# Kernel optimization log

Hardware: AMD Instinct MI355X
Metric: run time of the kernel (lower is better)

## Reference

```python
import jax, jax.numpy as jnp
import numpy as np

IH, IW = 32, 32
HEADS = 8
DIM_HEAD = 32
INNER = HEADS * DIM_HEAD  # 256
INP = 256
OUP = 256
SCALE = DIM_HEAD ** -0.5


def _relative_index(ih, iw):
    # Reproduce the torch buffer computation (meshgrid indexing='ij').
    yy, xx = np.meshgrid(np.arange(ih), np.arange(iw), indexing='ij')
    coords = np.stack([yy.ravel(), xx.ravel()])            # [2, n]
    rel = coords[:, :, None] - coords[:, None, :]          # [2, n, n]
    rel[0] += ih - 1
    rel[1] += iw - 1
    rel[0] *= 2 * iw - 1
    idx = rel.sum(0).ravel()                               # [n*n]
    return jnp.asarray(idx, dtype=jnp.int32)


def setup_inputs() -> dict:
    key = jax.random.key(0)
    k1, k2, k3, k4 = jax.random.split(key, 4)
    B, N = 16, IH * IW
    x = jax.random.normal(k1, (B, N, INP), dtype=jnp.float32)
    # Parameters (stored as [in, out] so forward is x @ W).
    W_qkv = jax.random.normal(k2, (INP, 3 * INNER), dtype=jnp.float32) * 0.02
    W_out = jax.random.normal(k3, (INNER, OUP), dtype=jnp.float32) * 0.02
    b_out = jnp.zeros((OUP,), dtype=jnp.float32)
    bias_table = jax.random.normal(k4, ((2 * IH - 1) * (2 * IW - 1), HEADS), dtype=jnp.float32) * 0.02
    rel_index = _relative_index(IH, IW)
    return {"x": x, "W_qkv": W_qkv, "W_out": W_out, "b_out": b_out,
            "bias_table": bias_table, "rel_index": rel_index}


def reference(x, W_qkv, W_out, b_out, bias_table, rel_index):
    B, N, _ = x.shape
    qkv = x @ W_qkv                                        # [B, N, 3*inner]
    q, k, v = jnp.split(qkv, 3, axis=-1)
    def to_heads(t):  # b n (h d) -> b h n d
        return t.reshape(B, N, HEADS, DIM_HEAD).transpose(0, 2, 1, 3)
    q, k, v = to_heads(q), to_heads(k), to_heads(v)
    dots = jnp.einsum('bhnd,bhmd->bhnm', q, k) * SCALE     # [B, H, N, N]
    # Gather relative position bias: [n*n, heads] -> [1, heads, n, n]
    rel_bias = bias_table[rel_index].reshape(N, N, HEADS).transpose(2, 0, 1)
    dots = dots + rel_bias[None]
    attn = jax.nn.softmax(dots, axis=-1)
    out = jnp.einsum('bhnm,bhmd->bhnd', attn, v)           # [B, H, N, D]
    out = out.transpose(0, 2, 1, 3).reshape(B, N, INNER)   # b n (h d)
    return out @ W_out + b_out
```

## Files before the change

kernel.cpp:

```cpp
#include <hip/hip_runtime.h>
#include <stdint.h>
#include <stddef.h>


typedef _Float16 f16;
typedef __attribute__((ext_vector_type(8))) _Float16 half8;
typedef __attribute__((ext_vector_type(4))) _Float16 half4;
typedef __attribute__((ext_vector_type(2))) __fp16 fp16x2;
typedef __attribute__((ext_vector_type(4))) float f32x4;

#define MFMA16(a, b, c) __builtin_amdgcn_mfma_f32_16x16x32_f16((a), (b), (c), 0, 0, 0)

__global__ __launch_bounds__(256) void prep_kernel(
    const float* __restrict__ x,
    const float* __restrict__ W_qkv, const float* __restrict__ W_out,
    const float* __restrict__ bias_table, const int* __restrict__ rel_index,
    f16* __restrict__ Wtq, f16* __restrict__ Wto, f16* __restrict__ ebC,
    f16* __restrict__ xh)
{
  (void)rel_index;
  const float kLog2e = 1.4426950408889634f;
  const float kScale = 0.17677669529663687f * kLog2e;
  int tid = blockIdx.x * 256 + threadIdx.x;
  if (tid < 24576) {
    int c = tid >> 5;
    int k8 = (tid & 31) << 3;
    float s = (c < 256) ? kScale : 1.0f;
    f16* dst = Wtq + c * 256 + k8;
#pragma unroll
    for (int j = 0; j < 8; ++j)
      dst[j] = (f16)(W_qkv[(k8 + j) * 768 + c] * s);
  } else if (tid < 32768) {
    int t = tid - 24576;
    int c = t >> 5;
    int k8 = (t & 31) << 3;
    f16* dst = Wto + c * 256 + k8;
#pragma unroll
    for (int j = 0; j < 8; ++j)
      dst[j] = (f16)W_out[(k8 + j) * 256 + c];
  } else if (tid < 97280) {
    int t = tid - 32768;
    int e = t * 8;
    int h = e / 64512;
    int r = e - h * 64512;
    int dy = r >> 10;
    int xi = (r >> 5) & 31;
    int xj0 = r & 31;
    int base = dy * 63 + xi + 31;
    f16* dst = ebC + e;
#pragma unroll
    for (int j = 0; j < 8; ++j)
      dst[j] = (f16)__expf(bias_table[(base - (xj0 + j)) * 8 + h]);
  } else {
    int t = tid - 97280;
    const float* src = x + (size_t)t * 8;
    f16* dst = xh + (size_t)t * 8;
#pragma unroll
    for (int j = 0; j < 8; ++j) dst[j] = (f16)src[j];
  }
}

__global__ __launch_bounds__(256, 4) void qkv_kernel(
    const f16* __restrict__ xh, const f16* __restrict__ Wt,
    f16* __restrict__ Qh, f16* __restrict__ Kh, f16* __restrict__ Vt)
{
  __shared__ f16 Bs[64 * 256];
  int mt = blockIdx.x, nt = blockIdx.y;
  int tid = threadIdx.x;
  int wave = tid >> 6, lane = tid & 63;
  int g = lane >> 4, q16 = lane & 15;
  int cbase = nt * 64;
  char* BsB = (char*)Bs;
  const f16* WtG = Wt + (size_t)cbase * 256;
#pragma unroll
  for (int i = 0; i < 8; ++i) {
    int c = i * 256 + tid;
    int row = c >> 5;
    int colb = (c & 31) << 4;
    half8 v = *(const half8*)(WtG + c * 8);
    *(half8*)(BsB + row * 512 + (colb ^ ((row & 7) << 4))) = v;
  }
  __syncthreads();

  int rbase = mt * 256 + wave * 64;
  const f16* xr0 = xh + (size_t)(rbase + q16) * 256 + g * 8;
  f32x4 acc[4][4] = {};
#pragma unroll 2
  for (int kc = 0; kc < 8; ++kc) {
    half8 bf[4];
#pragma unroll
    for (int cf = 0; cf < 4; ++cf) {
      int row = cf * 16 + q16;
      int colb = kc * 64 + g * 16;
      bf[cf] = *(const half8*)(BsB + row * 512 + (colb ^ ((row & 7) << 4)));
    }
#pragma unroll
    for (int mf = 0; mf < 4; ++mf) {
      half8 af = *(const half8*)(xr0 + (size_t)(mf * 16) * 256 + kc * 32);
#pragma unroll
      for (int cf = 0; cf < 4; ++cf)
        acc[mf][cf] = MFMA16(af, bf[cf], acc[mf][cf]);
    }
  }

#pragma unroll
  for (int mf = 0; mf < 4; ++mf) {
#pragma unroll
    for (int cf = 0; cf < 4; ++cf) {
      int c = cbase + cf * 16 + q16;
      int which = c >> 8, h = (c >> 5) & 7, d = c & 31;
      int m0 = rbase + mf * 16 + g * 4;
      int b = m0 >> 10, n0 = m0 & 1023;
      size_t bh = (size_t)(b * 8 + h);
      if (which == 2) {
        half4 vv;
#pragma unroll
        for (int r = 0; r < 4; ++r) vv[r] = (f16)acc[mf][cf][r];
        *(half4*)(Vt + (((bh << 5) | d) << 10) + n0) = vv;
      } else {
        f16* base = (which == 0) ? Qh : Kh;
#pragma unroll
        for (int r = 0; r < 4; ++r)
          base[((bh << 10) | (n0 + r)) * 32 + d] = (f16)acc[mf][cf][r];
      }
    }
  }
}

__global__ __launch_bounds__(256) void attn_kernel(
    const f16* __restrict__ Qh, const f16* __restrict__ Kh,
    const f16* __restrict__ Vt, const f16* __restrict__ ebC,
    f16* __restrict__ Oh)
{
  int bid = blockIdx.x;
  int h = bid & 7;
  int rest = bid >> 3;
  int qt = rest & 3;
  int b = rest >> 2;
  int wave = threadIdx.x >> 6, lane = threadIdx.x & 63;
  int g = lane >> 4, q16 = lane & 15;
  int bh = b * 8 + h;
  int qbase = qt * 256 + wave * 64;
  const f16* Qb = Qh + ((size_t)bh << 15);
  const f16* Kb = Kh + ((size_t)bh << 15);
  const f16* Vb = Vt + ((size_t)bh << 15);

  half8 qf0 = *(const half8*)(Qb + (size_t)(qbase +  0 + q16) * 32 + g * 8);
  half8 qf1 = *(const half8*)(Qb + (size_t)(qbase + 16 + q16) * 32 + g * 8);
  half8 qf2 = *(const half8*)(Qb + (size_t)(qbase + 32 + q16) * 32 + g * 8);
  half8 qf3 = *(const half8*)(Qb + (size_t)(qbase + 48 + q16) * 32 + g * 8);

  int kr0 = ((q16 >> 2) << 3) | (q16 & 3);
  const f16* Kp0 = Kb + kr0 * 32 + g * 8;
  const f16* Kp1 = Kp0 + 4 * 32;
  const f16* Vp0 = Vb + (size_t)q16 * 1024 + g * 8;
  const f16* Vp1 = Vb + (size_t)(16 + q16) * 1024 + g * 8;
  int yi0 = qbase >> 5;
  const f16* Bp = ebC + ((((h * 63 + yi0 + 31) * 32 + q16) << 5) + g * 8);

  f32x4 o0a = {0.f,0.f,0.f,0.f}, o1a = {0.f,0.f,0.f,0.f};
  f32x4 o0b = {0.f,0.f,0.f,0.f}, o1b = {0.f,0.f,0.f,0.f};
  f32x4 o0c = {0.f,0.f,0.f,0.f}, o1c = {0.f,0.f,0.f,0.f};
  f32x4 o0d = {0.f,0.f,0.f,0.f}, o1d = {0.f,0.f,0.f,0.f};
  float lsa = 0.f, lsb = 0.f, lsc = 0.f, lsd = 0.f;
  const fp16x2 one2 = {(__fp16)1.0f, (__fp16)1.0f};
  (void)one2;

#if __has_builtin(__builtin_amdgcn_fdot2)
#define LSUM(LS, PU)                                                         \
    LS = __builtin_amdgcn_fdot2(PU.h2[0], one2, LS, false);                  \
    LS = __builtin_amdgcn_fdot2(PU.h2[1], one2, LS, false);                  \
    LS = __builtin_amdgcn_fdot2(PU.h2[2], one2, LS, false);                  \
    LS = __builtin_amdgcn_fdot2(PU.h2[3], one2, LS, false);
#else
#define LSUM(LS, PU)                                                         \
    _Pragma("unroll") for (int i = 0; i < 8; ++i) { LS += (float)PU.h8[i]; }
#endif

#define FRAG_BODY(QF, K0, K1, V0, V1, EB, O0, O1, LS)                        \
  {                                                                          \
    const f32x4 zz = {0.f, 0.f, 0.f, 0.f};                                   \
    f32x4 s0 = MFMA16(K0, QF, zz);              \
    f32x4 s1 = MFMA16(K1, QF, zz);                         \
    union { fp16x2 h2[4]; half8 h8; } pu, eu;                                \
    eu.h8 = EB;                                                              \
    pu.h2[0] = __builtin_amdgcn_cvt_pkrtz(                                   \
        __builtin_amdgcn_exp2f(s0[0]), __builtin_amdgcn_exp2f(s0[1]));       \
    pu.h2[1] = __builtin_amdgcn_cvt_pkrtz(                                   \
        __builtin_amdgcn_exp2f(s0[2]), __builtin_amdgcn_exp2f(s0[3]));       \
    pu.h2[2] = __builtin_amdgcn_cvt_pkrtz(                                   \
        __builtin_amdgcn_exp2f(s1[0]), __builtin_amdgcn_exp2f(s1[1]));       \
    pu.h2[3] = __builtin_amdgcn_cvt_pkrtz(                                   \
        __builtin_amdgcn_exp2f(s1[2]), __builtin_amdgcn_exp2f(s1[3]));       \
    pu.h2[0] *= eu.h2[0];  pu.h2[1] *= eu.h2[1];           \
    pu.h2[2] *= eu.h2[2];  pu.h2[3] *= eu.h2[3];                             \
    LSUM(LS, pu)                                                             \
    O0 = MFMA16(V0, pu.h8, O0);                          \
    O1 = MFMA16(V1, pu.h8, O1);                       \
  }

  half8 kA0 = *(const half8*)Kp0;
  half8 kA1 = *(const half8*)Kp1;
  half8 vA0 = *(const half8*)Vp0;
  half8 vA1 = *(const half8*)Vp1;
  half8 bA0 = *(const half8*)(Bp);
  half8 bA1 = *(const half8*)(Bp + 512);
  half8 bA2 = *(const half8*)(Bp + 1024);
  half8 bA3 = *(const half8*)(Bp + 1536);

  for (int kt = 0; kt < 31; ++kt) {
    size_t ko = (size_t)(kt + 1) * 1024;
    int    co = (kt + 1) * 32;
    const f16* Bn = Bp - ko;
    half8 kB0 = *(const half8*)(Kp0 + ko);
    half8 kB1 = *(const half8*)(Kp1 + ko);
    half8 vB0 = *(const half8*)(Vp0 + co);
    half8 vB1 = *(const half8*)(Vp1 + co);
    half8 bB0 = *(const half8*)(Bn);
    half8 bB1 = *(const half8*)(Bn + 512);
    half8 bB2 = *(const half8*)(Bn + 1024);
    half8 bB3 = *(const half8*)(Bn + 1536);
    FRAG_BODY(qf0, kA0, kA1, vA0, vA1, bA0, o0a, o1a, lsa);
    FRAG_BODY(qf1, kA0, kA1, vA0, vA1, bA1, o0b, o1b, lsb);
    FRAG_BODY(qf2, kA0, kA1, vA0, vA1, bA2, o0c, o1c, lsc);
    FRAG_BODY(qf3, kA0, kA1, vA0, vA1, bA3, o0d, o1d, lsd);
    kA0 = kB0; kA1 = kB1; vA0 = vB0; vA1 = vB1;
    bA0 = bB0; bA1 = bB1; bA2 = bB2; bA3 = bB3;
  }
  FRAG_BODY(qf0, kA0, kA1, vA0, vA1, bA0, o0a, o1a, lsa);
  FRAG_BODY(qf1, kA0, kA1, vA0, vA1, bA1, o0b, o1b, lsb);
  FRAG_BODY(qf2, kA0, kA1, vA0, vA1, bA2, o0c, o1c, lsc);
  FRAG_BODY(qf3, kA0, kA1, vA0, vA1, bA3, o0d, o1d, lsd);
#undef FRAG_BODY
#undef LSUM

#define FRAG_OUT(O0, O1, LS, FOFF)                                           \
  {                                                                          \
    float l = LS;                                                            \
    l += __shfl_xor(l, 16);                                                  \
    l += __shfl_xor(l, 32);                                                  \
    float invl = 1.0f / l;                                                   \
    f16* op = Oh + (((size_t)bh << 10) + qbase + (FOFF) + q16) * 32;         \
    half4 w0, w1;                                                            \
    _Pragma("unroll") for (int r = 0; r < 4; ++r) {                          \
      w0[r] = (f16)(O0[r] * invl); w1[r] = (f16)(O1[r] * invl);              \
    }                                                                        \
    *(half4*)(op + g * 4) = w0;                                              \
    *(half4*)(op + 16 + g * 4) = w1;                                         \
  }
  FRAG_OUT(o0a, o1a, lsa, 0);
  FRAG_OUT(o0b, o1b, lsb, 16);
  FRAG_OUT(o0c, o1c, lsc, 32);
  FRAG_OUT(o0d, o1d, lsd, 48);
#undef FRAG_OUT
}

__global__ __launch_bounds__(256, 4) void out_kernel(
    const f16* __restrict__ Oh, const f16* __restrict__ Wto,
    const float* __restrict__ b_out, float* __restrict__ out)
{
  __shared__ f16 Bs[64 * 256];
  int mt = blockIdx.x, nt = blockIdx.y;
  int tid = threadIdx.x;
  int wave = tid >> 6, lane = tid & 63;
  int g = lane >> 4, q16 = lane & 15;
  int cbase = nt * 64;
  char* BsB = (char*)Bs;
  const f16* WtG = Wto + (size_t)cbase * 256;
#pragma unroll
  for (int i = 0; i < 8; ++i) {
    int c = i * 256 + tid;
    int row = c >> 5;
    int colb = (c & 31) << 4;
    half8 v = *(const half8*)(WtG + c * 8);
    *(half8*)(BsB + row * 512 + (colb ^ ((row & 7) << 4))) = v;
  }
  __syncthreads();

  int rbase = mt * 256 + wave * 64;
  int b = rbase >> 10;
  int nb = rbase & 1023;
  f32x4 acc[4][4] = {};
#pragma unroll 2
  for (int kc = 0; kc < 8; ++kc) {
    half8 bf[4];
#pragma unroll
    for (int cf = 0; cf < 4; ++cf) {
      int row = cf * 16 + q16;
      int colb = kc * 64 + g * 16;
      bf[cf] = *(const half8*)(BsB + row * 512 + (colb ^ ((row & 7) << 4)));
    }
#pragma unroll
    for (int mf = 0; mf < 4; ++mf) {
      int n = nb + mf * 16 + q16;
      half8 af = *(const half8*)(Oh + ((((size_t)(b * 8 + kc)) << 10) | n) * 32 + g * 8);
#pragma unroll
      for (int cf = 0; cf < 4; ++cf)
        acc[mf][cf] = MFMA16(af, bf[cf], acc[mf][cf]);
    }
  }

#pragma unroll
  for (int mf = 0; mf < 4; ++mf) {
#pragma unroll
    for (int cf = 0; cf < 4; ++cf) {
      int c = cbase + cf * 16 + q16;
      float bias = b_out[c];
#pragma unroll
      for (int r = 0; r < 4; ++r) {
        int mm = rbase + mf * 16 + g * 4 + r;
        out[(size_t)mm * 256 + c] = acc[mf][cf][r] + bias;
      }
    }
  }
}

extern "C" void kernel_launch(void* const* d_in, const int* in_sizes, int n_in,
                              void* d_out, int out_size, void* d_ws, size_t ws_size,
                              hipStream_t stream) {
  (void)in_sizes; (void)n_in; (void)out_size; (void)ws_size;
  const float* x        = (const float*)d_in[0];
  const float* W_qkv    = (const float*)d_in[1];
  const float* W_out    = (const float*)d_in[2];
  const float* b_out    = (const float*)d_in[3];
  const float* bias_tab = (const float*)d_in[4];
  const int*   rel_idx  = (const int*)d_in[5];
  float* out = (float*)d_out;
  char* ws = (char*)d_ws;

  f16* Qh  = (f16*)(ws);
  f16* Kh  = (f16*)(ws + (size_t)(8u  << 20));
  f16* Vt  = (f16*)(ws + (size_t)(16u << 20));
  f16* ebC = (f16*)(ws + (size_t)(24u << 20));
  f16* xh  = (f16*)(ws + (size_t)(40u << 20));
  f16* Oh  = (f16*)(ws + (size_t)(40u << 20));
  f16* Wtq = (f16*)(ws + (size_t)(48u << 20));
  f16* Wto = (f16*)(ws + (size_t)(48u << 20) + 768 * 256 * 2);

  hipLaunchKernelGGL(prep_kernel, dim3(2428), dim3(256), 0, stream,
                     x, W_qkv, W_out, bias_tab, rel_idx, Wtq, Wto, ebC, xh);
  hipLaunchKernelGGL(qkv_kernel, dim3(64, 12), dim3(256), 0, stream,
                     xh, Wtq, Qh, Kh, Vt);
  hipLaunchKernelGGL(attn_kernel, dim3(512), dim3(256), 0, stream,
                     Qh, Kh, Vt, ebC, Oh);
  hipLaunchKernelGGL(out_kernel, dim3(64, 4), dim3(256), 0, stream,
                     Oh, Wto, b_out, out);
}
```

Measured before the change: 80.67 us.

## Split attention key range in two blocks and merge partials in output projection

Each attention block now handles only half of the key tiles, and the grid doubles from 512 to 1024 blocks, so the GPU gets more concurrent work per CU. Each half writes unnormalised f16 partial outputs and per-row f32 exp-sum partials to the workspace. The output-projection kernel reads both partials, adds them, divides by the combined sum and feeds the result to the MFMAs. In exchange, the workspace traffic for the attention output roughly doubles and the output kernel does extra loads and arithmetic per A fragment.

```diff
diff --git a/kernel.cpp b/kernel.cpp
--- a/kernel.cpp
+++ b/kernel.cpp
@@ -10,6 +10,9 @@
 typedef __attribute__((ext_vector_type(4))) float f32x4;
 
 #define MFMA16(a, b, c) __builtin_amdgcn_mfma_f32_16x16x32_f16((a), (b), (c), 0, 0, 0)
+
+#define OHP_HALF  4194304u
+#define LP_HALF   131072u
 
 __global__ __launch_bounds__(256) void prep_kernel(
     const float* __restrict__ x,
@@ -130,17 +133,19 @@
 __global__ __launch_bounds__(256) void attn_kernel(
     const f16* __restrict__ Qh, const f16* __restrict__ Kh,
     const f16* __restrict__ Vt, const f16* __restrict__ ebC,
-    f16* __restrict__ Oh)
+    f16* __restrict__ OhP, float* __restrict__ lP)
 {
   int bid = blockIdx.x;
   int h = bid & 7;
   int rest = bid >> 3;
-  int qt = rest & 3;
-  int b = rest >> 2;
+  int half = rest & 1;
+  int qt = (rest >> 1) & 3;
+  int b = rest >> 3;
   int wave = threadIdx.x >> 6, lane = threadIdx.x & 63;
   int g = lane >> 4, q16 = lane & 15;
   int bh = b * 8 + h;
   int qbase = qt * 256 + wave * 64;
+  int kt0 = half << 4;
   const f16* Qb = Qh + ((size_t)bh << 15);
   const f16* Kb = Kh + ((size_t)bh << 15);
   const f16* Vb = Vt + ((size_t)bh << 15);
@@ -151,12 +156,13 @@
   half8 qf3 = *(const half8*)(Qb + (size_t)(qbase + 48 + q16) * 32 + g * 8);
 
   int kr0 = ((q16 >> 2) << 3) | (q16 & 3);
-  const f16* Kp0 = Kb + kr0 * 32 + g * 8;
+  const f16* Kp0 = Kb + kr0 * 32 + g * 8 + (size_t)kt0 * 1024;
   const f16* Kp1 = Kp0 + 4 * 32;
-  const f16* Vp0 = Vb + (size_t)q16 * 1024 + g * 8;
-  const f16* Vp1 = Vb + (size_t)(16 + q16) * 1024 + g * 8;
+  const f16* Vp0 = Vb + (size_t)q16 * 1024 + g * 8 + kt0 * 32;
+  const f16* Vp1 = Vb + (size_t)(16 + q16) * 1024 + g * 8 + kt0 * 32;
   int yi0 = qbase >> 5;
-  const f16* Bp = ebC + ((((h * 63 + yi0 + 31) * 32 + q16) << 5) + g * 8);
+  const f16* Bp = ebC + ((((h * 63 + yi0 + 31) * 32 + q16) << 5) + g * 8)
+                - (size_t)kt0 * 1024;
 
   f32x4 o0a = {0.f,0.f,0.f,0.f}, o1a = {0.f,0.f,0.f,0.f};
   f32x4 o0b = {0.f,0.f,0.f,0.f}, o1b = {0.f,0.f,0.f,0.f};
@@ -208,7 +214,7 @@
   half8 bA2 = *(const half8*)(Bp + 1024);
   half8 bA3 = *(const half8*)(Bp + 1536);
 
-  for (int kt = 0; kt < 31; ++kt) {
+  for (int kt = 0; kt < 15; ++kt) {
     size_t ko = (size_t)(kt + 1) * 1024;
     int    co = (kt + 1) * 32;
     const f16* Bn = Bp - ko;
@@ -239,14 +245,16 @@
     float l = LS;                                                            \
     l += __shfl_xor(l, 16);                                                  \
     l += __shfl_xor(l, 32);                                                  \
-    float invl = 1.0f / l;                                                   \
-    f16* op = Oh + (((size_t)bh << 10) + qbase + (FOFF) + q16) * 32;         \
+    int row = qbase + (FOFF) + q16;                                          \
+    f16* op = OhP + (size_t)half * OHP_HALF                                  \
+            + (((size_t)bh << 10) + row) * 32;                               \
     half4 w0, w1;                                                            \
     _Pragma("unroll") for (int r = 0; r < 4; ++r) {                          \
-      w0[r] = (f16)(O0[r] * invl); w1[r] = (f16)(O1[r] * invl);              \
+      w0[r] = (f16)O0[r]; w1[r] = (f16)O1[r];                                \
     }                                                                        \
     *(half4*)(op + g * 4) = w0;                                              \
     *(half4*)(op + 16 + g * 4) = w1;                                         \
+    if (g == 0) lP[half * LP_HALF + (bh << 10) + row] = l;                   \
   }
   FRAG_OUT(o0a, o1a, lsa, 0);
   FRAG_OUT(o0b, o1b, lsb, 16);
@@ -256,7 +264,8 @@
 }
 
 __global__ __launch_bounds__(256, 4) void out_kernel(
-    const f16* __restrict__ Oh, const f16* __restrict__ Wto,
+    const f16* __restrict__ OhP, const float* __restrict__ lP,
+    const f16* __restrict__ Wto,
     const float* __restrict__ b_out, float* __restrict__ out)
 {
   __shared__ f16 Bs[64 * 256];
@@ -293,7 +302,15 @@
 #pragma unroll
     for (int mf = 0; mf < 4; ++mf) {
       int n = nb + mf * 16 + q16;
-      half8 af = *(const half8*)(Oh + ((((size_t)(b * 8 + kc)) << 10) | n) * 32 + g * 8);
+      int ln = ((b * 8 + kc) << 10) | n;
+      size_t idx = (size_t)ln * 32 + g * 8;
+      half8 a0 = *(const half8*)(OhP + idx);
+      half8 a1 = *(const half8*)(OhP + OHP_HALF + idx);
+      float invl = 1.0f / (lP[ln] + lP[LP_HALF + ln]);
+      half8 af;
+#pragma unroll
+      for (int j = 0; j < 8; ++j)
+        af[j] = (f16)(((float)a0[j] + (float)a1[j]) * invl);
 #pragma unroll
       for (int cf = 0; cf < 4; ++cf)
         acc[mf][cf] = MFMA16(af, bf[cf], acc[mf][cf]);
@@ -328,21 +345,22 @@
   float* out = (float*)d_out;
   char* ws = (char*)d_ws;
 
-  f16* Qh  = (f16*)(ws);
-  f16* Kh  = (f16*)(ws + (size_t)(8u  << 20));
-  f16* Vt  = (f16*)(ws + (size_t)(16u << 20));
-  f16* ebC = (f16*)(ws + (size_t)(24u << 20));
-  f16* xh  = (f16*)(ws + (size_t)(40u << 20));
-  f16* Oh  = (f16*)(ws + (size_t)(40u << 20));
-  f16* Wtq = (f16*)(ws + (size_t)(48u << 20));
-  f16* Wto = (f16*)(ws + (size_t)(48u << 20) + 768 * 256 * 2);
+  f16*   Qh  = (f16*)(ws);
+  f16*   Kh  = (f16*)(ws + (size_t)(8u  << 20));
+  f16*   Vt  = (f16*)(ws + (size_t)(16u << 20));
+  f16*   ebC = (f16*)(ws + (size_t)(24u << 20));
+  f16*   OhP = (f16*)(ws + (size_t)(26u << 20));
+  float* lP  = (float*)(ws + (size_t)(42u << 20));
+  f16*   xh  = (f16*)(ws + (size_t)(40u << 20));
+  f16*   Wtq = (f16*)(ws + (size_t)(48u << 20));
+  f16*   Wto = (f16*)(ws + (size_t)(48u << 20) + 768 * 256 * 2);
 
   hipLaunchKernelGGL(prep_kernel, dim3(2428), dim3(256), 0, stream,
                      x, W_qkv, W_out, bias_tab, rel_idx, Wtq, Wto, ebC, xh);
   hipLaunchKernelGGL(qkv_kernel, dim3(64, 12), dim3(256), 0, stream,
                      xh, Wtq, Qh, Kh, Vt);
-  hipLaunchKernelGGL(attn_kernel, dim3(512), dim3(256), 0, stream,
-                     Qh, Kh, Vt, ebC, Oh);
+  hipLaunchKernelGGL(attn_kernel, dim3(1024), dim3(256), 0, stream,
+                     Qh, Kh, Vt, ebC, OhP, lP);
   hipLaunchKernelGGL(out_kernel, dim3(64, 4), dim3(256), 0, stream,
-                     Oh, Wto, b_out, out);
-}
+                     OhP, lP, Wto, b_out, out);
+}
```

Result: slower. 111.3 us (+37.9%).
